# Optimization experiments

Measured on AMD Instinct MI355X. Metric: run time of the kernel, lower is better.

## Reference

```python
import jax, jax.numpy as jnp
import numpy as np

V, E, T_MAX, H, L = 20000, 384, 512, 8, 8
D = E // H  # head size 48
FF = 4 * E


def setup_inputs() -> dict:
    key = jax.random.key(0)
    ks = jax.random.split(key, 24)
    B, T = 16, 512
    s = 0.02
    return {
        "index": jax.random.randint(ks[0], (B, T), 0, V, dtype=jnp.int64),
        "targets": jax.random.randint(ks[1], (B, T), 0, V, dtype=jnp.int64),
        "tok_emb": s * jax.random.normal(ks[2], (V, E), jnp.float32),
        "pos_emb": s * jax.random.normal(ks[3], (T_MAX, E), jnp.float32),
        "Wq": s * jax.random.normal(ks[4], (L, E, H, D), jnp.float32),
        "bq": jnp.zeros((L, H, D), jnp.float32),
        "Wk": s * jax.random.normal(ks[5], (L, E, H, D), jnp.float32),
        "bk": jnp.zeros((L, H, D), jnp.float32),
        "Wv": s * jax.random.normal(ks[6], (L, E, H, D), jnp.float32),
        "bv": jnp.zeros((L, H, D), jnp.float32),
        "Wo": s * jax.random.normal(ks[7], (L, E, E), jnp.float32),
        "bo": jnp.zeros((L, E), jnp.float32),
        "ln1_g": jnp.ones((L, E), jnp.float32),
        "ln1_b": jnp.zeros((L, E), jnp.float32),
        "ln2_g": jnp.ones((L, E), jnp.float32),
        "ln2_b": jnp.zeros((L, E), jnp.float32),
        "W1": s * jax.random.normal(ks[8], (L, E, FF), jnp.float32),
        "b1": jnp.zeros((L, FF), jnp.float32),
        "W2": s * jax.random.normal(ks[9], (L, FF, E), jnp.float32),
        "b2": jnp.zeros((L, E), jnp.float32),
        "lnf_g": jnp.ones((E,), jnp.float32),
        "lnf_b": jnp.zeros((E,), jnp.float32),
        "lm_b": jnp.zeros((V,), jnp.float32),
    }


def layernorm(x, g, b, eps=1e-5):
    mu = jnp.mean(x, axis=-1, keepdims=True)
    var = jnp.var(x, axis=-1, keepdims=True)
    return (x - mu) * jax.lax.rsqrt(var + eps) * g + b


def reference(index, targets, tok_emb, pos_emb, Wq, bq, Wk, bk, Wv, bv, Wo, bo,
              ln1_g, ln1_b, ln2_g, ln2_b, W1, b1, W2, b2, lnf_g, lnf_b, lm_b):
    B, T = index.shape
    x = tok_emb[index] + pos_emb[:T]  # [B,T,E]
    causal = jnp.tril(jnp.ones((T, T), bool))
    scale = D ** -0.5
    for l in range(L):
        h = layernorm(x, ln1_g[l], ln1_b[l])
        q = jnp.einsum('bte,ehd->bthd', h, Wq[l]) + bq[l]
        k = jnp.einsum('bte,ehd->bthd', h, Wk[l]) + bk[l]
        v = jnp.einsum('bte,ehd->bthd', h, Wv[l]) + bv[l]
        scores = jnp.einsum('bqhd,bkhd->bhqk', q, k) * scale
        scores = jnp.where(causal, scores, -jnp.inf)
        w = jax.nn.softmax(scores, axis=-1)
        attn = jnp.einsum('bhqk,bkhd->bqhd', w, v).reshape(B, T, E)
        x = x + attn @ Wo[l] + bo[l]
        h2 = layernorm(x, ln2_g[l], ln2_b[l])
        ff = jax.nn.gelu(h2 @ W1[l] + b1[l], approximate=False) @ W2[l] + b2[l]
        x = x + ff
    x = layernorm(x, lnf_g, lnf_b)
    logits = x @ tok_emb.T + lm_b  # tied weights
    logits = logits.reshape(B * T, V)
    logp = jax.nn.log_softmax(logits, axis=-1)
    loss = -jnp.mean(jnp.take_along_axis(logp, targets.reshape(-1, 1), axis=-1))
    return logits, loss
```

## Files before the change

### kernel.cpp

```cpp
#include <hip/hip_runtime.h>
#include <hip/hip_bf16.h>
#include <math.h>

#define M_ROWS 8192
#define E_DIM 384
#define FF_DIM 1536
#define V_DIM 20000
#define VPAD 20096
#define N_LAYER 8
#define QK_SCALE 0.14433756729740643f
#define PSTRIDE 160
#define NPART 157

typedef __bf16 bf16x8 __attribute__((ext_vector_type(8)));
typedef short  s16x8  __attribute__((ext_vector_type(8)));
typedef float  f32x4  __attribute__((ext_vector_type(4)));
typedef __hip_bfloat16 bf16_t;

__device__ __forceinline__ void gl2lds16(const void* g, void* l) {
    __builtin_amdgcn_global_load_lds((const __attribute__((address_space(1))) void*)g,
                                     (__attribute__((address_space(3))) void*)l, 16, 0, 0);
}
__device__ __forceinline__ unsigned short bf16bits(float v) {
    return __builtin_bit_cast(unsigned short, __float2bfloat16(v));
}

__global__ __launch_bounds__(256) void tconv_kernel(
    const float* __restrict__ in, bf16_t* __restrict__ out,
    int K, int N, int outRows, int rowoff)
{
    __shared__ float tile[32][33];
    const int n0 = blockIdx.x * 32, k0 = blockIdx.y * 32;
    const float* ip = in + (size_t)blockIdx.z * K * N;
    bf16_t* op = out + (size_t)blockIdx.z * outRows * K;
    const int tx = threadIdx.x & 31, ty = threadIdx.x >> 5;
#pragma unroll
    for (int i = 0; i < 32; i += 8)
        tile[ty + i][tx] = ip[(size_t)(k0 + ty + i) * N + n0 + tx];
    __syncthreads();
#pragma unroll
    for (int i = 0; i < 32; i += 8)
        op[(size_t)(rowoff + n0 + ty + i) * K + k0 + tx] = __float2bfloat16(tile[tx][ty + i]);
}

__global__ __launch_bounds__(256) void tokconv_kernel(
    const float* __restrict__ tok, bf16_t* __restrict__ out)
{
    const int total = VPAD * 48;
    for (int idx = blockIdx.x * 256 + threadIdx.x; idx < total; idx += gridDim.x * 256) {
        int row = idx / 48, gc = idx - row * 48;
        int col = gc * 8;
        s16x8 pk = {};
        if (row < V_DIM) {
            const float* tp = tok + (size_t)row * E_DIM + col;
            float4 f0 = *(const float4*)tp;
            float4 f1 = *(const float4*)(tp + 4);
            pk[0] = (short)bf16bits(f0.x); pk[1] = (short)bf16bits(f0.y);
            pk[2] = (short)bf16bits(f0.z); pk[3] = (short)bf16bits(f0.w);
            pk[4] = (short)bf16bits(f1.x); pk[5] = (short)bf16bits(f1.y);
            pk[6] = (short)bf16bits(f1.z); pk[7] = (short)bf16bits(f1.w);
        }
        *(s16x8*)&out[(size_t)row * E_DIM + col] = pk;
    }
}

__global__ __launch_bounds__(256) void bqkv_kernel(
    const float* __restrict__ bq, const float* __restrict__ bk,
    const float* __restrict__ bv, float* __restrict__ o)
{
    int i = blockIdx.x * 256 + threadIdx.x;
    if (i < N_LAYER * 1152) {
        int l = i / 1152, c = i - l * 1152;
        float v = (c < 384) ? bq[l * 384 + c] : (c < 768) ? bk[l * 384 + c - 384] : bv[l * 384 + c - 768];
        o[i] = v;
    }
}

__global__ __launch_bounds__(256) void embed_kernel(
    const int* __restrict__ idx, const float* __restrict__ tok,
    const float* __restrict__ pos, float* __restrict__ x)
{
    int row = blockIdx.x * 4 + (threadIdx.x >> 6);
    int lane = threadIdx.x & 63;
    int t = row & 511;
    int id = idx[row];
    const float* tr = tok + (size_t)id * E_DIM;
    const float* pr = pos + (size_t)t * E_DIM;
    float* xr = x + (size_t)row * E_DIM;
#pragma unroll
    for (int i = 0; i < 6; i++) { int c = lane + i * 64; xr[c] = tr[c] + pr[c]; }
}

__global__ __launch_bounds__(256) void ln_kernel(
    const float* __restrict__ x, const float* __restrict__ g,
    const float* __restrict__ b, bf16_t* __restrict__ out)
{
    int row = blockIdx.x * 4 + (threadIdx.x >> 6);
    int lane = threadIdx.x & 63;
    const float* xr = x + (size_t)row * E_DIM;
    float vals[6];
    float s = 0.f;
#pragma unroll
    for (int i = 0; i < 6; i++) { vals[i] = xr[lane + i * 64]; s += vals[i]; }
#pragma unroll
    for (int off = 1; off < 64; off <<= 1) s += __shfl_xor(s, off);
    float mu = s * (1.f / E_DIM);
    float sq = 0.f;
#pragma unroll
    for (int i = 0; i < 6; i++) { float d = vals[i] - mu; sq += d * d; }
#pragma unroll
    for (int off = 1; off < 64; off <<= 1) sq += __shfl_xor(sq, off);
    float rstd = rsqrtf(sq * (1.f / E_DIM) + 1e-5f);
    bf16_t* orow = out + (size_t)row * E_DIM;
#pragma unroll
    for (int i = 0; i < 6; i++) {
        int c = lane + i * 64;
        orow[c] = __float2bfloat16((vals[i] - mu) * rstd * g[c] + b[c]);
    }
}

template <int MODE, int MREP>
__global__ __launch_bounds__(256) void gemm_kernel(
    const bf16_t* __restrict__ A, const bf16_t* __restrict__ Bt,
    const float* __restrict__ bias, void* __restrict__ Cv, void* __restrict__ C2,
    int Ncols, int K)
{
    constexpr int BMR = MREP * 32;
    constexpr int ASH = BMR * 32;
    constexpr int BUFSH = ASH + 4096;
    constexpr int NLD = MREP / 2 + 2;
    __shared__ __align__(16) short smem[3 * BUFSH];
    const int t = threadIdx.x;
    const int w = t >> 6, lane = t & 63;
    const int wm = w >> 1, wn = w & 1;
    const int bm = blockIdx.y * BMR;
    const int bn = blockIdx.x * 128;

    f32x4 acc[MREP][4];
#pragma unroll
    for (int m = 0; m < MREP; m++)
#pragma unroll
        for (int n = 0; n < 4; n++)
            acc[m][n] = (f32x4){0.f, 0.f, 0.f, 0.f};

    const int lg = lane >> 4;
    const int ll = lane & 15;
    const int nt = K / 32;

    auto stagef = [&](int kt, int buf) {
        short* sA = smem + buf * BUFSH;
        short* sB = sA + ASH;
#pragma unroll
        for (int i = 0; i < MREP / 2; i++) {
            int li = i * 256 + t;
            int g = li >> (MREP == 4 ? 7 : 6);
            int row = li & (BMR - 1);
            gl2lds16(A + (size_t)(bm + row) * K + kt + g * 8,
                     sA + (size_t)(i * 256 + w * 64) * 8);
        }
#pragma unroll
        for (int i = 0; i < 2; i++) {
            int li = i * 256 + t;
            gl2lds16(Bt + (size_t)(bn + (li & 127)) * K + kt + (li >> 7) * 8,
                     sB + (size_t)(i * 256 + w * 64) * 8);
        }
    };

    stagef(0, 0);
    stagef(32, 1);

    for (int tt = 0; tt < nt; ++tt) {
        if (tt + 2 < nt) {
            stagef((tt + 2) * 32, (tt + 2) % 3);
            asm volatile("s_waitcnt vmcnt(%0)" :: "n"(2 * NLD) : "memory");
        } else if (tt + 1 < nt) {
            asm volatile("s_waitcnt vmcnt(%0)" :: "n"(NLD) : "memory");
        } else {
            asm volatile("s_waitcnt vmcnt(0)" ::: "memory");
        }
        __builtin_amdgcn_s_barrier();

        const short* sA = smem + (tt % 3) * BUFSH;
        const short* sB = sA + ASH;
        bf16x8 af[MREP], bfr[4];
#pragma unroll
        for (int m = 0; m < MREP; m++)
            af[m] = __builtin_bit_cast(bf16x8,
                *(const s16x8*)&sA[(lg * BMR + wm * (BMR / 2) + m * 16 + ll) * 8]);
#pragma unroll
        for (int n = 0; n < 4; n++)
            bfr[n] = __builtin_bit_cast(bf16x8,
                *(const s16x8*)&sB[(lg * 128 + wn * 64 + n * 16 + ll) * 8]);
#pragma unroll
        for (int m = 0; m < MREP; m++)
#pragma unroll
            for (int n = 0; n < 4; n++)
                acc[m][n] = __builtin_amdgcn_mfma_f32_16x16x32_bf16(bfr[n], af[m], acc[m][n], 0, 0, 0);

        __builtin_amdgcn_s_barrier();
    }

    const int rowm0 = bm + wm * (BMR / 2) + ll;
    const int coln0 = bn + wn * 64 + lg * 4;

    if constexpr (MODE == 4) {
        if (bn < 768) {
            bf16_t* qkvb = (bf16_t*)Cv;
            const float sc = (bn >= 384) ? 1.f : QK_SCALE;
#pragma unroll
            for (int n = 0; n < 4; n++) {
                const int coln = coln0 + n * 16;
                const float4 b4 = *(const float4*)&bias[coln];
#pragma unroll
                for (int m = 0; m < MREP; m++) {
                    const int row = rowm0 + m * 16;
                    ushort4 pk;
                    pk.x = bf16bits((acc[m][n][0] + b4.x) * sc);
                    pk.y = bf16bits((acc[m][n][1] + b4.y) * sc);
                    pk.z = bf16bits((acc[m][n][2] + b4.z) * sc);
                    pk.w = bf16bits((acc[m][n][3] + b4.w) * sc);
                    *(ushort4*)&qkvb[(size_t)row * 1152 + coln] = pk;
                }
            }
        } else {
            bf16_t* vtb = (bf16_t*)C2;
            const int cc0 = coln0 - 768;
#pragma unroll
            for (int n = 0; n < 4; n++) {
                const float4 b4 = *(const float4*)&bias[coln0 + n * 16];
#pragma unroll
                for (int m = 0; m < MREP; m++) {
                    const int row = rowm0 + m * 16;
                    const int bb = row >> 9, tt2 = row & 511;
                    bf16_t* vb = vtb + (size_t)bb * 384 * 512 + tt2;
                    vb[(size_t)(cc0 + n * 16 + 0) * 512] = __float2bfloat16(acc[m][n][0] + b4.x);
                    vb[(size_t)(cc0 + n * 16 + 1) * 512] = __float2bfloat16(acc[m][n][1] + b4.y);
                    vb[(size_t)(cc0 + n * 16 + 2) * 512] = __float2bfloat16(acc[m][n][2] + b4.z);
                    vb[(size_t)(cc0 + n * 16 + 3) * 512] = __float2bfloat16(acc[m][n][3] + b4.w);
                }
            }
        }
    } else if constexpr (MODE == 1) {
        float* C = (float*)Cv;
#pragma unroll
        for (int n = 0; n < 4; n++) {
            const int coln = coln0 + n * 16;
            const float4 b4 = *(const float4*)&bias[coln];
#pragma unroll
            for (int m = 0; m < MREP; m++) {
                const int row = rowm0 + m * 16;
                float4 cv = *(float4*)&C[(size_t)row * Ncols + coln];
                cv.x += acc[m][n][0] + b4.x;
                cv.y += acc[m][n][1] + b4.y;
                cv.z += acc[m][n][2] + b4.z;
                cv.w += acc[m][n][3] + b4.w;
                *(float4*)&C[(size_t)row * Ncols + coln] = cv;
            }
        }
    } else if constexpr (MODE == 2) {
        bf16_t* O = (bf16_t*)Cv;
#pragma unroll
        for (int n = 0; n < 4; n++) {
            const int coln = coln0 + n * 16;
            const float4 b4 = *(const float4*)&bias[coln];
#pragma unroll
            for (int m = 0; m < MREP; m++) {
                const int row = rowm0 + m * 16;
                float v0 = acc[m][n][0] + b4.x, v1 = acc[m][n][1] + b4.y;
                float v2 = acc[m][n][2] + b4.z, v3 = acc[m][n][3] + b4.w;
                v0 = 0.5f * v0 * (1.f + erff(v0 * 0.70710678118654752f));
                v1 = 0.5f * v1 * (1.f + erff(v1 * 0.70710678118654752f));
                v2 = 0.5f * v2 * (1.f + erff(v2 * 0.70710678118654752f));
                v3 = 0.5f * v3 * (1.f + erff(v3 * 0.70710678118654752f));
                ushort4 pk;
                pk.x = bf16bits(v0); pk.y = bf16bits(v1);
                pk.z = bf16bits(v2); pk.w = bf16bits(v3);
                *(ushort4*)&O[(size_t)row * Ncols + coln] = pk;
            }
        }
    }
}

__global__ __launch_bounds__(256) void logits_kernel(
    const bf16_t* __restrict__ A, const bf16_t* __restrict__ Bt,
    const float* __restrict__ bias, float* __restrict__ C,
    float* __restrict__ pbuf)
{
    __shared__ __align__(16) short smem[3 * 4096];
    const int t = threadIdx.x;
    const int w = t >> 6, lane = t & 63;
    const int lg = lane >> 4, ll = lane & 15;
    const int bm = blockIdx.x * 128;
    const int wr = bm + w * 32;
    const int tstart = (blockIdx.y * 157) >> 3;
    const int tend = ((blockIdx.y + 1) * 157) >> 3;

    bf16x8 af[12][2];
#pragma unroll
    for (int kt = 0; kt < 12; kt++)
#pragma unroll
        for (int m = 0; m < 2; m++)
            af[kt][m] = __builtin_bit_cast(bf16x8,
                *(const s16x8*)(A + (size_t)(wr + m * 16 + ll) * E_DIM + kt * 32 + lg * 8));

    auto stageB = [&](int tile, int kt, int buf) {
        short* sB = smem + buf * 4096;
#pragma unroll
        for (int i = 0; i < 2; i++) {
            int li = i * 256 + t;
            gl2lds16(Bt + (size_t)(tile * 128 + (li & 127)) * E_DIM + kt * 32 + (li >> 7) * 8,
                     sB + (size_t)(i * 256 + w * 64) * 8);
        }
    };

    stageB(tstart, 0, 0);
    stageB(tstart, 1, 1);

    for (int tile = tstart; tile < tend; ++tile) {
        f32x4 acc[2][8];
#pragma unroll
        for (int m = 0; m < 2; m++)
#pragma unroll
            for (int n = 0; n < 8; n++)
                acc[m][n] = (f32x4){0.f, 0.f, 0.f, 0.f};

#pragma unroll
        for (int kt = 0; kt < 12; ++kt) {
            const int sleft = (tend - 1 - tile) * 12 + (11 - kt);
            if (kt + 2 < 12) {
                stageB(tile, kt + 2, (kt + 2) % 3);
                asm volatile("s_waitcnt vmcnt(4)" ::: "memory");
            } else if (tile + 1 < tend) {
                stageB(tile + 1, kt + 2 - 12, (kt + 2) % 3);
                asm volatile("s_waitcnt vmcnt(4)" ::: "memory");
            } else if (sleft >= 1) {
                asm volatile("s_waitcnt vmcnt(2)" ::: "memory");
            } else {
                asm volatile("s_waitcnt vmcnt(0)" ::: "memory");
            }
            __builtin_amdgcn_s_barrier();

            const short* sB = smem + (kt % 3) * 4096;
            bf16x8 bfr[8];
#pragma unroll
            for (int n = 0; n < 8; n++)
                bfr[n] = __builtin_bit_cast(bf16x8,
                    *(const s16x8*)&sB[(lg * 128 + n * 16 + ll) * 8]);
#pragma unroll
            for (int m = 0; m < 2; m++)
#pragma unroll
                for (int n = 0; n < 8; n++)
                    acc[m][n] = __builtin_amdgcn_mfma_f32_16x16x32_bf16(
                        bfr[n], af[kt][m], acc[m][n], 0, 0, 0);

            __builtin_amdgcn_s_barrier();
        }

        const int tc = tile * 128;
#pragma unroll
        for (int m = 0; m < 2; m++) {
            const int row = wr + m * 16 + ll;
            float se = 0.f;
#pragma unroll
            for (int n = 0; n < 8; n++) {
                const int coln = tc + n * 16 + lg * 4;
                if (coln + 3 < V_DIM) {
                    const float4 b4 = *(const float4*)&bias[coln];
                    f32x4 v;
                    v[0] = acc[m][n][0] + b4.x;
                    v[1] = acc[m][n][1] + b4.y;
                    v[2] = acc[m][n][2] + b4.z;
                    v[3] = acc[m][n][3] + b4.w;
                    __builtin_nontemporal_store(v, (f32x4*)&C[(size_t)row * V_DIM + coln]);
                    se += __expf(v[0]) + __expf(v[1]) + __expf(v[2]) + __expf(v[3]);
                } else {
#pragma unroll
                    for (int e = 0; e < 4; e++) {
                        int col = coln + e;
                        if (col < V_DIM) {
                            float v = acc[m][n][e] + bias[col];
                            __builtin_nontemporal_store(v, &C[(size_t)row * V_DIM + col]);
                            se += __expf(v);
                        }
                    }
                }
            }
            se += __shfl_xor(se, 16);
            se += __shfl_xor(se, 32);
            if (lg == 0)
                __builtin_nontemporal_store(se, &pbuf[(size_t)row * PSTRIDE + tile]);
        }
    }
}

__global__ __launch_bounds__(256) void attn_kernel(
    const bf16_t* __restrict__ qkvb, const bf16_t* __restrict__ vt,
    bf16_t* __restrict__ o)
{
    const int bh = blockIdx.y;
    const int b = bh >> 3, h = bh & 7;
    __shared__ unsigned short psm[4608];
    const int tid = threadIdx.x;
    const int w = tid >> 6, lane = tid & 63;
    const int ll = lane & 15, g = lane >> 4;

    const bf16_t* kptr = qkvb + (size_t)b * 512 * 1152 + 384 + h * 48;
    const bf16_t* vptr = vt + (size_t)b * 384 * 512 + (size_t)h * 48 * 512;

    auto runQ = [&](int qt) {
        const int q0 = qt * 64;
        const int q_abs = q0 + ll * 4 + w;

        const bf16_t* qrow = qkvb + (size_t)(b * 512 + q_abs) * 1152 + h * 48;
        bf16x8 qf0 = __builtin_bit_cast(bf16x8, *(const s16x8*)(qrow + g * 8));
        bf16x8 qf1 = {};
        if (g < 2) qf1 = __builtin_bit_cast(bf16x8, *(const s16x8*)(qrow + 32 + g * 8));

        f32x4 oacc[3];
#pragma unroll
        for (int df = 0; df < 3; df++) oacc[df] = (f32x4){0.f, 0.f, 0.f, 0.f};
        float ssum = 0.f;
        const int ntiles = 2 * (qt + 1);

        auto loadK = [&](int kbase, bf16x8& c00, bf16x8& c01, bf16x8& c10, bf16x8& c11) {
            const bf16_t* kr0 = kptr + (size_t)(kbase + ll) * 1152;
            const bf16_t* kr1 = kptr + (size_t)(kbase + 16 + ll) * 1152;
            c00 = __builtin_bit_cast(bf16x8, *(const s16x8*)(kr0 + g * 8));
            c10 = __builtin_bit_cast(bf16x8, *(const s16x8*)(kr1 + g * 8));
            bf16x8 z = {};
            c01 = (g < 2) ? __builtin_bit_cast(bf16x8, *(const s16x8*)(kr0 + 32 + g * 8)) : z;
            c11 = (g < 2) ? __builtin_bit_cast(bf16x8, *(const s16x8*)(kr1 + 32 + g * 8)) : z;
        };

        auto doTile = [&](int kbase, int parity,
                          const bf16x8& c00, const bf16x8& c01, const bf16x8& c10, const bf16x8& c11,
                          bool pf, int nbase,
                          bf16x8& n00, bf16x8& n01, bf16x8& n10, bf16x8& n11) {
            bf16x8 vf[3];
#pragma unroll
            for (int df = 0; df < 3; df++)
                vf[df] = __builtin_bit_cast(bf16x8,
                    *(const s16x8*)(vptr + (size_t)(df * 16 + ll) * 512 + kbase + g * 8));
            if (pf) loadK(nbase, n00, n01, n10, n11);

            f32x4 sfr[2];
            {
                f32x4 z0 = {0.f, 0.f, 0.f, 0.f};
                z0 = __builtin_amdgcn_mfma_f32_16x16x32_bf16(c00, qf0, z0, 0, 0, 0);
                z0 = __builtin_amdgcn_mfma_f32_16x16x32_bf16(c01, qf1, z0, 0, 0, 0);
                sfr[0] = z0;
                f32x4 z1 = {0.f, 0.f, 0.f, 0.f};
                z1 = __builtin_amdgcn_mfma_f32_16x16x32_bf16(c10, qf0, z1, 0, 0, 0);
                z1 = __builtin_amdgcn_mfma_f32_16x16x32_bf16(c11, qf1, z1, 0, 0, 0);
                sfr[1] = z1;
            }

            float p[8];
#pragma unroll
            for (int f = 0; f < 2; f++)
#pragma unroll
                for (int j = 0; j < 4; j++) {
                    int key = kbase + f * 16 + g * 4 + j;
                    float sv = sfr[f][j];
                    sv = (key > q_abs) ? -1e30f : sv;
                    float pv = __expf(fminf(sv, 20.f));
                    p[f * 4 + j] = pv;
                    ssum += pv;
                }

            const int pbase = (w * 2 + parity) * 576;
#pragma unroll
            for (int f = 0; f < 2; f++)
#pragma unroll
                for (int j = 0; j < 4; j++)
                    psm[pbase + (f * 16 + g * 4 + j) * 18 + ll] = bf16bits(p[f * 4 + j]);
            s16x8 pr;
#pragma unroll
            for (int i = 0; i < 8; i++)
                pr[i] = (short)psm[pbase + (g * 8 + i) * 18 + ll];
            bf16x8 pfr = __builtin_bit_cast(bf16x8, pr);
#pragma unroll
            for (int df = 0; df < 3; df++)
                oacc[df] = __builtin_amdgcn_mfma_f32_16x16x32_bf16(vf[df], pfr, oacc[df], 0, 0, 0);
        };

        bf16x8 kA0, kA1, kA2, kA3, kB0, kB1, kB2, kB3;
        loadK(0, kA0, kA1, kA2, kA3);
        for (int kt = 0; kt < ntiles; kt += 2) {
            doTile(kt * 32, 0, kA0, kA1, kA2, kA3,
                   true, (kt + 1) * 32, kB0, kB1, kB2, kB3);
            doTile((kt + 1) * 32, 1, kB0, kB1, kB2, kB3,
                   (kt + 2) < ntiles, (kt + 2) * 32, kA0, kA1, kA2, kA3);
        }

        ssum += __shfl_xor(ssum, 16);
        ssum += __shfl_xor(ssum, 32);
        float inv = 1.f / ssum;
        bf16_t* orow = o + (size_t)(b * 512 + q_abs) * 384 + h * 48;
#pragma unroll
        for (int df = 0; df < 3; df++) {
            ushort4 pk;
            pk.x = bf16bits(oacc[df][0] * inv);
            pk.y = bf16bits(oacc[df][1] * inv);
            pk.z = bf16bits(oacc[df][2] * inv);
            pk.w = bf16bits(oacc[df][3] * inv);
            *(ushort4*)&orow[df * 16 + g * 4] = pk;
        }
    };

    runQ(blockIdx.x);
    runQ(7 - blockIdx.x);
}

__global__ __launch_bounds__(256) void loss_row2_kernel(
    const float* __restrict__ pbuf, const float* __restrict__ logits,
    const int* __restrict__ targets, float* __restrict__ rowloss)
{
    int row = blockIdx.x * 4 + (threadIdx.x >> 6);
    int lane = threadIdx.x & 63;
    const float* pr = pbuf + (size_t)row * PSTRIDE;
    float s = 0.f;
    for (int i = lane; i < NPART; i += 64) s += pr[i];
#pragma unroll
    for (int off = 1; off < 64; off <<= 1) s += __shfl_xor(s, off);
    if (lane == 0) {
        int tgt = targets[row];
        rowloss[row] = logf(s) - logits[(size_t)row * V_DIM + tgt];
    }
}

__global__ __launch_bounds__(256) void loss_reduce_kernel(
    const float* __restrict__ rowloss, float* __restrict__ out)
{
    int t = threadIdx.x;
    __shared__ float red[4];
    float s = 0.f;
    for (int i = t; i < M_ROWS; i += 256) s += rowloss[i];
#pragma unroll
    for (int off = 1; off < 64; off <<= 1) s += __shfl_xor(s, off);
    if ((t & 63) == 0) red[t >> 6] = s;
    __syncthreads();
    if (t == 0) out[0] = (red[0] + red[1] + red[2] + red[3]) * (1.f / M_ROWS);
}

extern "C" void kernel_launch(void* const* d_in, const int* in_sizes, int n_in,
                              void* d_out, int out_size, void* d_ws, size_t ws_size,
                              hipStream_t stream)
{
    const int*   index   = (const int*)d_in[0];
    const int*   targets = (const int*)d_in[1];
    const float* tok_emb = (const float*)d_in[2];
    const float* pos_emb = (const float*)d_in[3];
    const float* Wq = (const float*)d_in[4];
    const float* bq = (const float*)d_in[5];
    const float* Wk = (const float*)d_in[6];
    const float* bk = (const float*)d_in[7];
    const float* Wv = (const float*)d_in[8];
    const float* bv = (const float*)d_in[9];
    const float* Wo = (const float*)d_in[10];
    const float* bo = (const float*)d_in[11];
    const float* ln1_g = (const float*)d_in[12];
    const float* ln1_b = (const float*)d_in[13];
    const float* ln2_g = (const float*)d_in[14];
    const float* ln2_b = (const float*)d_in[15];
    const float* W1 = (const float*)d_in[16];
    const float* b1 = (const float*)d_in[17];
    const float* W2 = (const float*)d_in[18];
    const float* b2 = (const float*)d_in[19];
    const float* lnf_g = (const float*)d_in[20];
    const float* lnf_b = (const float*)d_in[21];
    const float* lm_b  = (const float*)d_in[22];

    float* out = (float*)d_out;
    char* wsb = (char*)d_ws;

    float*  x     = (float*)(wsb + 0);
    bf16_t* hbuf  = (bf16_t*)(wsb + 12582912);
    bf16_t* obuf  = (bf16_t*)(wsb + 18874368);
    bf16_t* qkvb  = (bf16_t*)(wsb + 25165824);
    bf16_t* vtb   = (bf16_t*)(wsb + 44040192);
    bf16_t* ffmid = (bf16_t*)(wsb + 18874368);
    float*  pbuf  = (float*)(wsb + 25165824);
    bf16_t* tokb  = (bf16_t*)(wsb + 50331648);
    bf16_t* qkvw  = (bf16_t*)(wsb + 65765376);
    bf16_t* wo_t  = (bf16_t*)(wsb + 72843264);
    bf16_t* w1_t  = (bf16_t*)(wsb + 75202560);
    bf16_t* w2_t  = (bf16_t*)(wsb + 84639744);
    float*  bqkv  = (float*)(wsb + 94076928);
    float*  rowloss = (float*)(wsb + 94113792);

    tokconv_kernel<<<2048, 256, 0, stream>>>(tok_emb, tokb);
    tconv_kernel<<<dim3(12, 12, 8), 256, 0, stream>>>(Wq, qkvw, 384, 384, 1152, 0);
    tconv_kernel<<<dim3(12, 12, 8), 256, 0, stream>>>(Wk, qkvw, 384, 384, 1152, 384);
    tconv_kernel<<<dim3(12, 12, 8), 256, 0, stream>>>(Wv, qkvw, 384, 384, 1152, 768);
    tconv_kernel<<<dim3(12, 12, 8), 256, 0, stream>>>(Wo, wo_t, 384, 384, 384, 0);
    tconv_kernel<<<dim3(48, 12, 8), 256, 0, stream>>>(W1, w1_t, 384, 1536, 1536, 0);
    tconv_kernel<<<dim3(12, 48, 8), 256, 0, stream>>>(W2, w2_t, 1536, 384, 384, 0);
    bqkv_kernel<<<36, 256, 0, stream>>>(bq, bk, bv, bqkv);

    embed_kernel<<<2048, 256, 0, stream>>>(index, tok_emb, pos_emb, x);

    for (int l = 0; l < N_LAYER; l++) {
        const bf16_t* qkvw_l = qkvw + (size_t)l * 1152 * 384;
        const float*  bqkv_l = bqkv + l * 1152;
        ln_kernel<<<2048, 256, 0, stream>>>(x, ln1_g + l * E_DIM, ln1_b + l * E_DIM, hbuf);
        gemm_kernel<4, 4><<<dim3(9, 64), 256, 0, stream>>>(
            hbuf, qkvw_l, bqkv_l, qkvb, vtb, 1152, 384);
        attn_kernel<<<dim3(4, 128), 256, 0, stream>>>(qkvb, vtb, obuf);
        gemm_kernel<1, 2><<<dim3(3, 128), 256, 0, stream>>>(
            obuf, wo_t + (size_t)l * 384 * 384, bo + l * E_DIM, x, nullptr, 384, 384);
        ln_kernel<<<2048, 256, 0, stream>>>(x, ln2_g + l * E_DIM, ln2_b + l * E_DIM, hbuf);
        gemm_kernel<2, 4><<<dim3(12, 64), 256, 0, stream>>>(
            hbuf, w1_t + (size_t)l * 1536 * 384, b1 + l * FF_DIM, ffmid, nullptr, 1536, 384);
        gemm_kernel<1, 2><<<dim3(3, 128), 256, 0, stream>>>(
            ffmid, w2_t + (size_t)l * 384 * 1536, b2 + l * E_DIM, x, nullptr, 384, 1536);
    }

    ln_kernel<<<2048, 256, 0, stream>>>(x, lnf_g, lnf_b, hbuf);
    logits_kernel<<<dim3(64, 8), 256, 0, stream>>>(hbuf, tokb, lm_b, out, pbuf);

    loss_row2_kernel<<<2048, 256, 0, stream>>>(pbuf, out, targets, rowloss);
    loss_reduce_kernel<<<1, 256, 0, stream>>>(rowloss, out + (size_t)M_ROWS * V_DIM);
}
```

Measured before the change: 1.641 ms.

## Fuse LayerNorm into QKV, FFN-up and logits GEMMs via row-resident sweep kernel

Removes the standalone LayerNorm kernels and computes LN inside the consumer GEMMs. A new sweep kernel keeps each wave's 16 rows of normalized activations in registers as bf16 fragments and streams several 128-column weight tiles through a 3-buffer LDS pipeline. The logits kernel likewise normalizes its rows from fp32 x directly. This saves the hbuf write and re-read plus kernel launches, at the cost of higher register pressure and a different tiling (64-row blocks with weight reuse only across 4 waves).

```diff
diff --git a/kernel.cpp b/kernel.cpp
--- a/kernel.cpp
+++ b/kernel.cpp
@@ -91,34 +91,6 @@
     for (int i = 0; i < 6; i++) { int c = lane + i * 64; xr[c] = tr[c] + pr[c]; }
 }
 
-__global__ __launch_bounds__(256) void ln_kernel(
-    const float* __restrict__ x, const float* __restrict__ g,
-    const float* __restrict__ b, bf16_t* __restrict__ out)
-{
-    int row = blockIdx.x * 4 + (threadIdx.x >> 6);
-    int lane = threadIdx.x & 63;
-    const float* xr = x + (size_t)row * E_DIM;
-    float vals[6];
-    float s = 0.f;
-#pragma unroll
-    for (int i = 0; i < 6; i++) { vals[i] = xr[lane + i * 64]; s += vals[i]; }
-#pragma unroll
-    for (int off = 1; off < 64; off <<= 1) s += __shfl_xor(s, off);
-    float mu = s * (1.f / E_DIM);
-    float sq = 0.f;
-#pragma unroll
-    for (int i = 0; i < 6; i++) { float d = vals[i] - mu; sq += d * d; }
-#pragma unroll
-    for (int off = 1; off < 64; off <<= 1) sq += __shfl_xor(sq, off);
-    float rstd = rsqrtf(sq * (1.f / E_DIM) + 1e-5f);
-    bf16_t* orow = out + (size_t)row * E_DIM;
-#pragma unroll
-    for (int i = 0; i < 6; i++) {
-        int c = lane + i * 64;
-        orow[c] = __float2bfloat16((vals[i] - mu) * rstd * g[c] + b[c]);
-    }
-}
-
 template <int MODE, int MREP>
 __global__ __launch_bounds__(256) void gemm_kernel(
     const bf16_t* __restrict__ A, const bf16_t* __restrict__ Bt,
@@ -203,44 +175,7 @@
     const int rowm0 = bm + wm * (BMR / 2) + ll;
     const int coln0 = bn + wn * 64 + lg * 4;
 
-    if constexpr (MODE == 4) {
-        if (bn < 768) {
-            bf16_t* qkvb = (bf16_t*)Cv;
-            const float sc = (bn >= 384) ? 1.f : QK_SCALE;
-#pragma unroll
-            for (int n = 0; n < 4; n++) {
-                const int coln = coln0 + n * 16;
-                const float4 b4 = *(const float4*)&bias[coln];
-#pragma unroll
-                for (int m = 0; m < MREP; m++) {
-                    const int row = rowm0 + m * 16;
-                    ushort4 pk;
-                    pk.x = bf16bits((acc[m][n][0] + b4.x) * sc);
-                    pk.y = bf16bits((acc[m][n][1] + b4.y) * sc);
-                    pk.z = bf16bits((acc[m][n][2] + b4.z) * sc);
-                    pk.w = bf16bits((acc[m][n][3] + b4.w) * sc);
-                    *(ushort4*)&qkvb[(size_t)row * 1152 + coln] = pk;
-                }
-            }
-        } else {
-            bf16_t* vtb = (bf16_t*)C2;
-            const int cc0 = coln0 - 768;
-#pragma unroll
-            for (int n = 0; n < 4; n++) {
-                const float4 b4 = *(const float4*)&bias[coln0 + n * 16];
-#pragma unroll
-                for (int m = 0; m < MREP; m++) {
-                    const int row = rowm0 + m * 16;
-                    const int bb = row >> 9, tt2 = row & 511;
-                    bf16_t* vb = vtb + (size_t)bb * 384 * 512 + tt2;
-                    vb[(size_t)(cc0 + n * 16 + 0) * 512] = __float2bfloat16(acc[m][n][0] + b4.x);
-                    vb[(size_t)(cc0 + n * 16 + 1) * 512] = __float2bfloat16(acc[m][n][1] + b4.y);
-                    vb[(size_t)(cc0 + n * 16 + 2) * 512] = __float2bfloat16(acc[m][n][2] + b4.z);
-                    vb[(size_t)(cc0 + n * 16 + 3) * 512] = __float2bfloat16(acc[m][n][3] + b4.w);
-                }
-            }
-        }
-    } else if constexpr (MODE == 1) {
+    if constexpr (MODE == 1) {
         float* C = (float*)Cv;
 #pragma unroll
         for (int n = 0; n < 4; n++) {
@@ -257,34 +192,155 @@
                 *(float4*)&C[(size_t)row * Ncols + coln] = cv;
             }
         }
-    } else if constexpr (MODE == 2) {
-        bf16_t* O = (bf16_t*)Cv;
-#pragma unroll
-        for (int n = 0; n < 4; n++) {
-            const int coln = coln0 + n * 16;
-            const float4 b4 = *(const float4*)&bias[coln];
-#pragma unroll
-            for (int m = 0; m < MREP; m++) {
-                const int row = rowm0 + m * 16;
-                float v0 = acc[m][n][0] + b4.x, v1 = acc[m][n][1] + b4.y;
-                float v2 = acc[m][n][2] + b4.z, v3 = acc[m][n][3] + b4.w;
-                v0 = 0.5f * v0 * (1.f + erff(v0 * 0.70710678118654752f));
-                v1 = 0.5f * v1 * (1.f + erff(v1 * 0.70710678118654752f));
-                v2 = 0.5f * v2 * (1.f + erff(v2 * 0.70710678118654752f));
-                v3 = 0.5f * v3 * (1.f + erff(v3 * 0.70710678118654752f));
+    }
+}
+
+template <int MODE, int SWEEP>
+__global__ __launch_bounds__(256) void sweep_kernel(
+    const float* __restrict__ X, const float* __restrict__ lng, const float* __restrict__ lnb,
+    const bf16_t* __restrict__ Bt, const float* __restrict__ bias,
+    bf16_t* __restrict__ O, bf16_t* __restrict__ vtb)
+{
+    constexpr int NCOLS = (MODE == 4) ? 1152 : 1536;
+    __shared__ __align__(16) short smem[3 * 4096];
+    const int t = threadIdx.x;
+    const int w = t >> 6, lane = t & 63;
+    const int lg = lane >> 4, ll = lane & 15;
+    const int row = blockIdx.x * 64 + w * 16 + ll;
+    const int tstart = blockIdx.y * SWEEP;
+
+    auto stageB = [&](int tile, int kt, int buf) {
+        short* sB = smem + buf * 4096;
+#pragma unroll
+        for (int i = 0; i < 2; i++) {
+            int li = i * 256 + t;
+            gl2lds16(Bt + (size_t)(tile * 128 + (li & 127)) * E_DIM + kt * 32 + (li >> 7) * 8,
+                     sB + (size_t)(i * 256 + w * 64) * 8);
+        }
+    };
+
+    stageB(tstart, 0, 0);
+    stageB(tstart, 1, 1);
+
+    float xv[12][8];
+    float sum = 0.f;
+#pragma unroll
+    for (int kt = 0; kt < 12; kt++) {
+        const float* xp = X + (size_t)row * E_DIM + kt * 32 + lg * 8;
+        float4 a0 = *(const float4*)xp;
+        float4 a1 = *(const float4*)(xp + 4);
+        xv[kt][0] = a0.x; xv[kt][1] = a0.y; xv[kt][2] = a0.z; xv[kt][3] = a0.w;
+        xv[kt][4] = a1.x; xv[kt][5] = a1.y; xv[kt][6] = a1.z; xv[kt][7] = a1.w;
+        sum += a0.x + a0.y + a0.z + a0.w + a1.x + a1.y + a1.z + a1.w;
+    }
+    sum += __shfl_xor(sum, 16);
+    sum += __shfl_xor(sum, 32);
+    const float mu = sum * (1.f / 384.f);
+    float sq = 0.f;
+#pragma unroll
+    for (int kt = 0; kt < 12; kt++)
+#pragma unroll
+        for (int e = 0; e < 8; e++) { float d = xv[kt][e] - mu; sq += d * d; }
+    sq += __shfl_xor(sq, 16);
+    sq += __shfl_xor(sq, 32);
+    const float rstd = rsqrtf(sq * (1.f / 384.f) + 1e-5f);
+
+    bf16x8 af[12];
+#pragma unroll
+    for (int kt = 0; kt < 12; kt++) {
+        const float* gp = lng + kt * 32 + lg * 8;
+        const float* bp = lnb + kt * 32 + lg * 8;
+        float4 g0 = *(const float4*)gp, g1 = *(const float4*)(gp + 4);
+        float4 b0 = *(const float4*)bp, b1 = *(const float4*)(bp + 4);
+        s16x8 pk;
+        pk[0] = (short)bf16bits((xv[kt][0] - mu) * rstd * g0.x + b0.x);
+        pk[1] = (short)bf16bits((xv[kt][1] - mu) * rstd * g0.y + b0.y);
+        pk[2] = (short)bf16bits((xv[kt][2] - mu) * rstd * g0.z + b0.z);
+        pk[3] = (short)bf16bits((xv[kt][3] - mu) * rstd * g0.w + b0.w);
+        pk[4] = (short)bf16bits((xv[kt][4] - mu) * rstd * g1.x + b1.x);
+        pk[5] = (short)bf16bits((xv[kt][5] - mu) * rstd * g1.y + b1.y);
+        pk[6] = (short)bf16bits((xv[kt][6] - mu) * rstd * g1.z + b1.z);
+        pk[7] = (short)bf16bits((xv[kt][7] - mu) * rstd * g1.w + b1.w);
+        af[kt] = __builtin_bit_cast(bf16x8, pk);
+    }
+
+    for (int ti = 0; ti < SWEEP; ++ti) {
+        const int tile = tstart + ti;
+        f32x4 acc[8];
+#pragma unroll
+        for (int n = 0; n < 8; n++) acc[n] = (f32x4){0.f, 0.f, 0.f, 0.f};
+
+#pragma unroll
+        for (int kt = 0; kt < 12; ++kt) {
+            const int sleft = (SWEEP - 1 - ti) * 12 + (11 - kt);
+            if (kt + 2 < 12) {
+                stageB(tile, kt + 2, (kt + 2) % 3);
+                asm volatile("s_waitcnt vmcnt(4)" ::: "memory");
+            } else if (ti + 1 < SWEEP) {
+                stageB(tile + 1, kt + 2 - 12, (kt + 2) % 3);
+                asm volatile("s_waitcnt vmcnt(4)" ::: "memory");
+            } else if (sleft >= 1) {
+                asm volatile("s_waitcnt vmcnt(2)" ::: "memory");
+            } else {
+                asm volatile("s_waitcnt vmcnt(0)" ::: "memory");
+            }
+            __builtin_amdgcn_s_barrier();
+
+            const short* sB = smem + (kt % 3) * 4096;
+            bf16x8 bfr[8];
+#pragma unroll
+            for (int n = 0; n < 8; n++)
+                bfr[n] = __builtin_bit_cast(bf16x8,
+                    *(const s16x8*)&sB[(lg * 128 + n * 16 + ll) * 8]);
+#pragma unroll
+            for (int n = 0; n < 8; n++)
+                acc[n] = __builtin_amdgcn_mfma_f32_16x16x32_bf16(bfr[n], af[kt], acc[n], 0, 0, 0);
+
+            __builtin_amdgcn_s_barrier();
+        }
+
+        if (MODE == 2 || tile < 6) {
+            const float sc = (MODE == 4 && tile < 3) ? QK_SCALE : 1.f;
+#pragma unroll
+            for (int n = 0; n < 8; n++) {
+                const int coln = tile * 128 + n * 16 + lg * 4;
+                const float4 b4 = *(const float4*)&bias[coln];
+                float v0 = acc[n][0] + b4.x, v1 = acc[n][1] + b4.y;
+                float v2 = acc[n][2] + b4.z, v3 = acc[n][3] + b4.w;
+                if (MODE == 2) {
+                    v0 = 0.5f * v0 * (1.f + erff(v0 * 0.70710678118654752f));
+                    v1 = 0.5f * v1 * (1.f + erff(v1 * 0.70710678118654752f));
+                    v2 = 0.5f * v2 * (1.f + erff(v2 * 0.70710678118654752f));
+                    v3 = 0.5f * v3 * (1.f + erff(v3 * 0.70710678118654752f));
+                } else {
+                    v0 *= sc; v1 *= sc; v2 *= sc; v3 *= sc;
+                }
                 ushort4 pk;
                 pk.x = bf16bits(v0); pk.y = bf16bits(v1);
                 pk.z = bf16bits(v2); pk.w = bf16bits(v3);
-                *(ushort4*)&O[(size_t)row * Ncols + coln] = pk;
+                *(ushort4*)&O[(size_t)row * NCOLS + coln] = pk;
             }
+        } else {
+            const int bb = row >> 9, tt2 = row & 511;
+            bf16_t* vb = vtb + (size_t)bb * 384 * 512 + tt2;
+#pragma unroll
+            for (int n = 0; n < 8; n++) {
+                const int coln = tile * 128 + n * 16 + lg * 4;
+                const float4 b4 = *(const float4*)&bias[coln];
+                const int cc = coln - 768;
+                vb[(size_t)(cc + 0) * 512] = __float2bfloat16(acc[n][0] + b4.x);
+                vb[(size_t)(cc + 1) * 512] = __float2bfloat16(acc[n][1] + b4.y);
+                vb[(size_t)(cc + 2) * 512] = __float2bfloat16(acc[n][2] + b4.z);
+                vb[(size_t)(cc + 3) * 512] = __float2bfloat16(acc[n][3] + b4.w);
+            }
         }
     }
 }
 
 __global__ __launch_bounds__(256) void logits_kernel(
-    const bf16_t* __restrict__ A, const bf16_t* __restrict__ Bt,
-    const float* __restrict__ bias, float* __restrict__ C,
-    float* __restrict__ pbuf)
+    const float* __restrict__ X, const float* __restrict__ lng, const float* __restrict__ lnb,
+    const bf16_t* __restrict__ Bt, const float* __restrict__ bias,
+    float* __restrict__ C, float* __restrict__ pbuf)
 {
     __shared__ __align__(16) short smem[3 * 4096];
     const int t = threadIdx.x;
@@ -295,14 +351,6 @@
     const int tstart = (blockIdx.y * 157) >> 3;
     const int tend = ((blockIdx.y + 1) * 157) >> 3;
 
-    bf16x8 af[12][2];
-#pragma unroll
-    for (int kt = 0; kt < 12; kt++)
-#pragma unroll
-        for (int m = 0; m < 2; m++)
-            af[kt][m] = __builtin_bit_cast(bf16x8,
-                *(const s16x8*)(A + (size_t)(wr + m * 16 + ll) * E_DIM + kt * 32 + lg * 8));
-
     auto stageB = [&](int tile, int kt, int buf) {
         short* sB = smem + buf * 4096;
 #pragma unroll
@@ -315,6 +363,51 @@
 
     stageB(tstart, 0, 0);
     stageB(tstart, 1, 1);
+
+    bf16x8 af[12][2];
+#pragma unroll
+    for (int m = 0; m < 2; m++) {
+        const int row = wr + m * 16 + ll;
+        float xv[12][8];
+        float sum = 0.f;
+#pragma unroll
+        for (int kt = 0; kt < 12; kt++) {
+            const float* xp = X + (size_t)row * E_DIM + kt * 32 + lg * 8;
+            float4 a0 = *(const float4*)xp;
+            float4 a1 = *(const float4*)(xp + 4);
+            xv[kt][0] = a0.x; xv[kt][1] = a0.y; xv[kt][2] = a0.z; xv[kt][3] = a0.w;
+            xv[kt][4] = a1.x; xv[kt][5] = a1.y; xv[kt][6] = a1.z; xv[kt][7] = a1.w;
+            sum += a0.x + a0.y + a0.z + a0.w + a1.x + a1.y + a1.z + a1.w;
+        }
+        sum += __shfl_xor(sum, 16);
+        sum += __shfl_xor(sum, 32);
+        const float mu = sum * (1.f / 384.f);
+        float sq = 0.f;
+#pragma unroll
+        for (int kt = 0; kt < 12; kt++)
+#pragma unroll
+            for (int e = 0; e < 8; e++) { float d = xv[kt][e] - mu; sq += d * d; }
+        sq += __shfl_xor(sq, 16);
+        sq += __shfl_xor(sq, 32);
+        const float rstd = rsqrtf(sq * (1.f / 384.f) + 1e-5f);
+#pragma unroll
+        for (int kt = 0; kt < 12; kt++) {
+            const float* gp = lng + kt * 32 + lg * 8;
+            const float* bp = lnb + kt * 32 + lg * 8;
+            float4 g0 = *(const float4*)gp, g1 = *(const float4*)(gp + 4);
+            float4 b0 = *(const float4*)bp, b1 = *(const float4*)(bp + 4);
+            s16x8 pk;
+            pk[0] = (short)bf16bits((xv[kt][0] - mu) * rstd * g0.x + b0.x);
+            pk[1] = (short)bf16bits((xv[kt][1] - mu) * rstd * g0.y + b0.y);
+            pk[2] = (short)bf16bits((xv[kt][2] - mu) * rstd * g0.z + b0.z);
+            pk[3] = (short)bf16bits((xv[kt][3] - mu) * rstd * g0.w + b0.w);
+            pk[4] = (short)bf16bits((xv[kt][4] - mu) * rstd * g1.x + b1.x);
+            pk[5] = (short)bf16bits((xv[kt][5] - mu) * rstd * g1.y + b1.y);
+            pk[6] = (short)bf16bits((xv[kt][6] - mu) * rstd * g1.z + b1.z);
+            pk[7] = (short)bf16bits((xv[kt][7] - mu) * rstd * g1.w + b1.w);
+            af[kt][m] = __builtin_bit_cast(bf16x8, pk);
+        }
+    }
 
     for (int tile = tstart; tile < tend; ++tile) {
         f32x4 acc[2][8];
@@ -575,7 +668,6 @@
     char* wsb = (char*)d_ws;
 
     float*  x     = (float*)(wsb + 0);
-    bf16_t* hbuf  = (bf16_t*)(wsb + 12582912);
     bf16_t* obuf  = (bf16_t*)(wsb + 18874368);
     bf16_t* qkvb  = (bf16_t*)(wsb + 25165824);
     bf16_t* vtb   = (bf16_t*)(wsb + 44040192);
@@ -603,21 +695,20 @@
     for (int l = 0; l < N_LAYER; l++) {
         const bf16_t* qkvw_l = qkvw + (size_t)l * 1152 * 384;
         const float*  bqkv_l = bqkv + l * 1152;
-        ln_kernel<<<2048, 256, 0, stream>>>(x, ln1_g + l * E_DIM, ln1_b + l * E_DIM, hbuf);
-        gemm_kernel<4, 4><<<dim3(9, 64), 256, 0, stream>>>(
-            hbuf, qkvw_l, bqkv_l, qkvb, vtb, 1152, 384);
+        sweep_kernel<4, 3><<<dim3(128, 3), 256, 0, stream>>>(
+            x, ln1_g + l * E_DIM, ln1_b + l * E_DIM, qkvw_l, bqkv_l, qkvb, vtb);
         attn_kernel<<<dim3(4, 128), 256, 0, stream>>>(qkvb, vtb, obuf);
         gemm_kernel<1, 2><<<dim3(3, 128), 256, 0, stream>>>(
             obuf, wo_t + (size_t)l * 384 * 384, bo + l * E_DIM, x, nullptr, 384, 384);
-        ln_kernel<<<2048, 256, 0, stream>>>(x, ln2_g + l * E_DIM, ln2_b + l * E_DIM, hbuf);
-        gemm_kernel<2, 4><<<dim3(12, 64), 256, 0, stream>>>(
-            hbuf, w1_t + (size_t)l * 1536 * 384, b1 + l * FF_DIM, ffmid, nullptr, 1536, 384);
+        sweep_kernel<2, 3><<<dim3(128, 4), 256, 0, stream>>>(
+            x, ln2_g + l * E_DIM, ln2_b + l * E_DIM,
+            w1_t + (size_t)l * 1536 * 384, b1 + l * FF_DIM, ffmid, nullptr);
         gemm_kernel<1, 2><<<dim3(3, 128), 256, 0, stream>>>(
             ffmid, w2_t + (size_t)l * 384 * 1536, b2 + l * E_DIM, x, nullptr, 384, 1536);
     }
 
-    ln_kernel<<<2048, 256, 0, stream>>>(x, lnf_g, lnf_b, hbuf);
-    logits_kernel<<<dim3(64, 8), 256, 0, stream>>>(hbuf, tokb, lm_b, out, pbuf);
+    logits_kernel<<<dim3(64, 8), 256, 0, stream>>>(
+        x, lnf_g, lnf_b, tokb, lm_b, out, pbuf);
 
     loss_row2_kernel<<<2048, 256, 0, stream>>>(pbuf, out, targets, rowloss);
     loss_reduce_kernel<<<1, 256, 0, stream>>>(rowloss, out + (size_t)M_ROWS * V_DIM);
```

Result: slower. 1.712 ms (+4.3%).
